# Kernel tuning notes

Hardware: AMD Instinct MI355X
Metric: run time of the kernel (lower is better)

## Reference

```python
import jax, jax.numpy as jnp
import numpy as np

W_LEN = 37  # window_length
EPS = 1e-9
LRELU_SLOPE = 0.2
SQRT2 = 1.4142135623730951


def win_sum(x, w):
    # Depthwise sliding-window sum of width w, 'same' padding w//2 (odd w).
    # Equivalent to the diag-kernel conv1d in the original code, but O(T) via cumsum.
    pad = w // 2
    xp = jnp.pad(x, ((0, 0), (0, 0), (pad, pad)))
    cs = jnp.cumsum(xp, axis=-1)
    cs = jnp.pad(cs, ((0, 0), (0, 0), (1, 0)))
    return cs[..., w:] - cs[..., :-w]


def conv1d(x, w, b):
    # x: [B,C,T], w: [O,I,3], padding=1
    y = jax.lax.conv_general_dilated(x, w, (1,), [(1, 1)],
                                     dimension_numbers=('NCH', 'OIH', 'NCH'))
    return y + b[None, :, None]


def adawin_instance(x, s, mask, fc_w, fc_b, alpha):
    # x: [B,C,T], s: [B,S,T], mask: [B,T]
    C = x.shape[1]
    h = jnp.einsum('bst,cs->bct', s, fc_w) + fc_b[None, :, None]  # [B,2C,T]
    m = mask[:, None, :]                       # [B,1,T]
    denom = win_sum(m, W_LEN) + EPS            # same for all channels
    gamma = win_sum(h[:, :C], W_LEN) / denom * m
    beta = win_sum(h[:, C:], W_LEN) / denom * m
    x_norm = jnp.tanh(alpha * x)               # WindowedNorm1d.forward
    return (1.0 + gamma) * x_norm + beta


def setup_inputs() -> dict:
    key = jax.random.key(0)
    ks = jax.random.split(key, 10)
    B, C_IN, C_OUT, S, T = 16, 512, 512, 128, 2048
    inp = {
        'x': jax.random.normal(ks[0], (B, C_IN, T), dtype=jnp.float32),
        's': jax.random.normal(ks[1], (B, S, T), dtype=jnp.float32),
        'lengths': jax.random.randint(ks[2], (B,), 0, T).astype(jnp.int32),
        'fc1_w': jax.random.normal(ks[3], (2 * C_IN, S), dtype=jnp.float32) * 0.05,
        'fc1_b': jnp.zeros((2 * C_IN,), dtype=jnp.float32),
        'alpha1': jnp.full((1,), 0.5, dtype=jnp.float32),
        'conv1_w': jax.random.normal(ks[4], (C_OUT, C_IN, 3), dtype=jnp.float32) * 0.02,
        'conv1_b': jnp.zeros((C_OUT,), dtype=jnp.float32),
        'fc2_w': jax.random.normal(ks[5], (2 * C_OUT, S), dtype=jnp.float32) * 0.05,
        'fc2_b': jnp.zeros((2 * C_OUT,), dtype=jnp.float32),
        'alpha2': jnp.full((1,), 0.5, dtype=jnp.float32),
        'conv2_w': jax.random.normal(ks[6], (C_OUT, C_OUT, 3), dtype=jnp.float32) * 0.02,
        'conv2_b': jnp.zeros((C_OUT,), dtype=jnp.float32),
    }
    return inp


def reference(x, s, lengths, fc1_w, fc1_b, alpha1, conv1_w, conv1_b,
              fc2_w, fc2_b, alpha2, conv2_w, conv2_b):
    T = x.shape[2]
    mask = (jnp.arange(T)[None, :] < lengths[:, None]).astype(x.dtype)  # [B,T]

    h = adawin_instance(x, s, mask, fc1_w, fc1_b, alpha1)
    h = jax.nn.leaky_relu(h, LRELU_SLOPE)
    h = conv1d(h, conv1_w, conv1_b)
    h = adawin_instance(h, s, mask, fc2_w, fc2_b, alpha2)
    h = jax.nn.leaky_relu(h, LRELU_SLOPE)
    h = conv1d(h, conv2_w, conv2_b)

    # dim_in == dim_out -> identity shortcut
    return (h + x) / SQRT2
```

## Files before the change

### kernel.cpp

```cpp
#include <hip/hip_runtime.h>

#define B_ 16
#define C_ 512
#define S_ 128
#define T_ 2048
#define HALF 18
#define WLEN 37

typedef __bf16 bf16x8 __attribute__((ext_vector_type(8)));
typedef float f32x4 __attribute__((ext_vector_type(4)));
typedef float f32x16 __attribute__((ext_vector_type(16)));
typedef unsigned short ushort_t;

__device__ inline ushort_t f2bf(float x) {
    unsigned u = __float_as_uint(x);
    u += 0x7fffu + ((u >> 16) & 1u);
    return (ushort_t)(u >> 16);
}
__device__ inline float bf2f(ushort_t h) {
    return __uint_as_float(((unsigned)h) << 16);
}
__device__ inline float fast_tanh(float z) {
    float e = __expf(2.f * z);
    return 1.f - __fdividef(2.f, e + 1.f);
}
__device__ __forceinline__ void glds16(const void* g, void* l) {
    __builtin_amdgcn_global_load_lds(
        (const __attribute__((address_space(1))) unsigned*)g,
        (__attribute__((address_space(3))) unsigned*)l, 16, 0, 0);
}

#define MFMA16(a, b, c) __builtin_amdgcn_mfma_f32_16x16x32_bf16((a), (b), (c), 0, 0, 0)
#define MFMA32(a, b, c) __builtin_amdgcn_mfma_f32_32x32x16_bf16((a), (b), (c), 0, 0, 0)

__global__ void prep_weights(const float* __restrict__ fc1, const float* __restrict__ fc2,
                             ushort_t* __restrict__ Wfc) {
    const int n_fc = 1024 * 128;
    int idx = blockIdx.x * blockDim.x + threadIdx.x;
    if (idx < n_fc) Wfc[idx] = f2bf(fc1[idx]);
    else if (idx < 2 * n_fc) Wfc[idx] = f2bf(fc2[idx - n_fc]);
}

#define IMGCH 53248
#define A_BYTES 53248
#define B_BYTES 22528
__global__ void prep_conv_images(const float* __restrict__ c1, const float* __restrict__ c2,
                                 ushort_t* __restrict__ I1, ushort_t* __restrict__ I2) {
    int idx = blockIdx.x * blockDim.x + threadIdx.x;
    const int per_conv = 2 * 16 * 256 * 13;
    if (idx >= 2 * per_conv) return;
    int conv = idx >= per_conv;
    int rr = conv ? idx - per_conv : idx;
    const float* src = conv ? c2 : c1;
    ushort_t* dst = conv ? I2 : I1;
    int imgchunk = rr / 3328;
    int rem = rr - imgchunk * 3328;
    int r = rem / 13;
    int g = rem - r * 13;
    int mb = imgchunk >> 4, ch = imgchunk & 15;
    ushort_t vals[8];
    if (g == 12) {
#pragma unroll
        for (int e = 0; e < 8; ++e) vals[e] = 0;
    } else {
        int tap = g >> 2, seg = g & 3;
        int o = mb * 256 + r;
        int chb = ch * 32 + seg * 8;
#pragma unroll
        for (int e = 0; e < 8; ++e)
            vals[e] = f2bf(src[(size_t)(o * 512 + chb + e) * 3 + tap]);
    }
    uint4 pk;
    pk.x = vals[0] | ((unsigned)vals[1] << 16);
    pk.y = vals[2] | ((unsigned)vals[3] << 16);
    pk.z = vals[4] | ((unsigned)vals[5] << 16);
    pk.w = vals[6] | ((unsigned)vals[7] << 16);
    *(uint4*)&dst[(size_t)rr * 8] = pk;
}

__global__ void zero_pads(ushort_t* __restrict__ y1p, ushort_t* __restrict__ y2p) {
    int tid = blockIdx.x * blockDim.x + threadIdx.x;
    if (tid < 4096) {
        ushort_t* base = (tid & 1) ? y2p : y1p;
        int r = tid >> 1;
        int bb = r >> 7;
        int rowsel = (r >> 6) & 1;
        int col = (r & 63) * 8;
        size_t row = (size_t)bb * (T_ + 2) + (rowsel ? (T_ + 1) : 0);
        *(uint4*)&base[row * C_ + col] = (uint4){0, 0, 0, 0};
    }
}

__global__ __launch_bounds__(256) void winsum_kernel(const float* __restrict__ s,
                                                     ushort_t* __restrict__ sw_t) {
    int b = blockIdx.y;
    int t0 = blockIdx.x * 64;
    __shared__ float sb[128][101];
    int tid = threadIdx.x;
    for (int e = tid; e < 128 * 100; e += 256) {
        int sj = e / 100;
        int u = e - sj * 100;
        int gt = t0 - HALF + u;
        float v = 0.f;
        if (gt >= 0 && gt < T_) v = s[((size_t)(b * S_ + sj)) * T_ + gt];
        sb[sj][u] = v;
    }
    __syncthreads();
    for (int e = tid; e < 64 * 128; e += 256) {
        int tl = e >> 7;
        int sj = e & 127;
        float sum = 0.f;
#pragma unroll
        for (int d = 0; d < WLEN; ++d) sum += sb[sj][tl + d];
        sw_t[((size_t)(b * T_ + t0 + tl)) * S_ + sj] = f2bf(sum);
    }
}

template <int INLAYOUT>
__global__ __launch_bounds__(256) void adawin_kernel(
    const void* __restrict__ xin_, const ushort_t* __restrict__ sw_t,
    const ushort_t* __restrict__ Wfc, const float* __restrict__ fcb,
    const float* __restrict__ alpha, const int* __restrict__ lengths,
    ushort_t* __restrict__ youtp) {
    int t0 = blockIdx.x * 64;
    int c0 = blockIdx.y * 64;
    int b = blockIdx.z;
    __shared__ __attribute__((aligned(16))) ushort_t smem[128 * 136 + 64 * 136];
    ushort_t (*As)[136] = (ushort_t(*)[136])smem;
    ushort_t (*Bs)[136] = (ushort_t(*)[136])(smem + 128 * 136);
    int tid = threadIdx.x;

    {
        int r = tid >> 4;
        int cseg = (tid & 15) * 8;
#pragma unroll
        for (int p = 0; p < 8; ++p) {
            int row = p * 16 + r;
            int grow = (row < 64) ? (c0 + row) : (448 + c0 + row);
            *(uint4*)&As[row][cseg] = *(const uint4*)&Wfc[(size_t)grow * 128 + cseg];
        }
    }
    {
        int tl = tid & 63;
        int sg = tid >> 6;
        const ushort_t* src = &sw_t[((size_t)(b * T_ + t0 + tl)) * S_];
#pragma unroll
        for (int j = 0; j < 4; ++j) {
            int col = sg * 32 + j * 8;
            *(uint4*)&Bs[tl][col] = *(const uint4*)&src[col];
        }
    }
    __syncthreads();

    int wave = tid >> 6, lane = tid & 63;
    int quad = lane >> 4, l = lane & 15;
    f32x4 accg[4], accb[4];
#pragma unroll
    for (int n = 0; n < 4; ++n) {
        accg[n] = (f32x4){0.f, 0.f, 0.f, 0.f};
        accb[n] = (f32x4){0.f, 0.f, 0.f, 0.f};
    }
    int rg = wave * 16 + l;
    int rb = 64 + wave * 16 + l;
#pragma unroll
    for (int ks = 0; ks < 4; ++ks) {
        int kc = ks * 32 + quad * 8;
        bf16x8 ag = *(const bf16x8*)&As[rg][kc];
        bf16x8 ab = *(const bf16x8*)&As[rb][kc];
#pragma unroll
        for (int n = 0; n < 4; ++n) {
            bf16x8 bb = *(const bf16x8*)&Bs[n * 16 + l][kc];
            accg[n] = MFMA16(ag, bb, accg[n]);
            accb[n] = MFMA16(ab, bb, accb[n]);
        }
    }

    __syncthreads();
    ushort_t (*Ts)[72] = (ushort_t(*)[72])smem;

    int len = lengths[b];
    float alph = alpha[0];
    const float* xf = (const float*)xin_;
    const ushort_t* xh = (const ushort_t*)xin_;
    int clocal = wave * 16 + quad * 4;
    int cbase = c0 + clocal;
#pragma unroll
    for (int n = 0; n < 4; ++n) {
        int t = t0 + n * 16 + l;
        int lo = t - HALF; if (lo < 0) lo = 0;
        int hi = t + HALF; if (hi > T_ - 1) hi = T_ - 1;
        float cnt = (float)(hi - lo + 1);
        int hv = hi < (len - 1) ? hi : (len - 1);
        int mdi = hv - lo + 1; if (mdi < 0) mdi = 0;
        float m = (t < len) ? 1.f : 0.f;
        float sc = m / ((float)mdi + 1e-9f);

        float xv[4];
        if (INLAYOUT == 0) {
#pragma unroll
            for (int j = 0; j < 4; ++j)
                xv[j] = xf[(size_t)(b * C_ + cbase + j) * T_ + t];
        } else {
            uint2 xraw = *(const uint2*)&xh[((size_t)(b * (T_ + 2) + 1 + t)) * C_ + cbase];
            xv[0] = bf2f((ushort_t)(xraw.x & 0xffff));
            xv[1] = bf2f((ushort_t)(xraw.x >> 16));
            xv[2] = bf2f((ushort_t)(xraw.y & 0xffff));
            xv[3] = bf2f((ushort_t)(xraw.y >> 16));
        }
        unsigned pk[2];
#pragma unroll
        for (int j = 0; j < 4; ++j) {
            int c = cbase + j;
            float gamma = (accg[n][j] + fcb[c] * cnt) * sc;
            float beta = (accb[n][j] + fcb[C_ + c] * cnt) * sc;
            float xn = fast_tanh(alph * xv[j]);
            float v = (1.f + gamma) * xn + beta;
            v = v > 0.f ? v : 0.2f * v;
            unsigned hv16 = (unsigned)f2bf(v);
            if (j & 1) pk[j >> 1] |= hv16 << 16;
            else pk[j >> 1] = hv16;
        }
        *(uint2*)&Ts[n * 16 + l][clocal] = (uint2){pk[0], pk[1]};
    }
    __syncthreads();
    {
        int row = tid >> 2;
        int seg = (tid & 3) * 16;
        size_t gbase = ((size_t)(b * (T_ + 2) + 1 + t0 + row)) * C_ + c0 + seg;
        *(uint4*)&youtp[gbase] = *(const uint4*)&Ts[row][seg];
        *(uint4*)&youtp[gbase + 8] = *(const uint4*)&Ts[row][seg + 8];
    }
}

__device__ __forceinline__ void issue_g(int g, const char* img, const char* xt, int ch,
                                        char* Ab, char* Bb, int lane) {
    if (g < 52) {
        glds16(img + g * 1024 + lane * 16, Ab + g * 1024);
    } else if (g < 74) {
        int j = g - 52;
        int gi = j * 64 + lane;
        int r = gi / 5;
        int gg = gi - r * 5;
        if (gg == 4) gg = 0;
        if (r > 257) r = 257;
        glds16(xt + (size_t)r * 1024 + ch * 64 + gg * 16, Bb + j * 1024);
    } else {
        int j = g - 74;
        glds16(img + j * 1024 + lane * 16, Ab + j * 1024);
    }
}
template <int G0, int G1>
__device__ __forceinline__ void issue_batch(const char* img, const char* xt, int ch,
                                            char* Ab, char* Bb, int wave, int lane) {
#pragma unroll
    for (int g = G0; g < G1; ++g) {
        if ((g & 7) != wave) continue;
        issue_g(g, img, xt, ch, Ab, Bb, lane);
    }
}

template <int EPI>
__global__ __launch_bounds__(512, 2) void conv_kernel(
    const ushort_t* __restrict__ Xp, const ushort_t* __restrict__ Wimg,
    const float* __restrict__ bias, const float* __restrict__ resid,
    ushort_t* __restrict__ out_bf, float* __restrict__ out_f) {
    int t0 = blockIdx.x * 256;
    int o0 = blockIdx.y * 256;
    int b = blockIdx.z;
    __shared__ __attribute__((aligned(16))) char smem[2 * A_BYTES + 2 * B_BYTES];
    int tid = threadIdx.x;
    int lane = tid & 63, wave = tid >> 6;
    int l32 = lane & 31, khalf = lane >> 5;
    int wm = wave >> 2, wn = wave & 3;

    const char* imgch = (const char*)Wimg + (size_t)blockIdx.y * 16 * IMGCH;
    const char* xt = (const char*)Xp + (size_t)(b * (T_ + 2) + t0) * 1024;

    f32x16 acc[4][2];
#pragma unroll
    for (int m = 0; m < 4; ++m)
#pragma unroll
        for (int nf = 0; nf < 2; ++nf)
#pragma unroll
            for (int r = 0; r < 16; ++r) acc[m][nf][r] = 0.f;

    char* A0 = smem;
    char* A1 = smem + A_BYTES;
    char* Bb0 = smem + 2 * A_BYTES;
    char* Bb1 = Bb0 + B_BYTES;

    issue_batch<0, 80>(imgch, xt, 0, A0, Bb0, wave, lane);
    issue_batch<0, 32>(imgch + IMGCH, xt, 1, A1, Bb1, wave, lane);
    asm volatile("s_waitcnt vmcnt(4)" ::: "memory");
    asm volatile("s_barrier" ::: "memory");

#pragma unroll 1
    for (int ch = 0; ch < 16; ++ch) {
        int cur = ch & 1;
        char* Ac = smem + cur * A_BYTES;
        char* Bc = smem + 2 * A_BYTES + cur * B_BYTES;
        char* An = smem + (cur ^ 1) * A_BYTES;
        char* Bn = smem + 2 * A_BYTES + (cur ^ 1) * B_BYTES;
        ushort_t (*As)[104] = (ushort_t(*)[104])Ac;
        ushort_t (*Bs)[40] = (ushort_t(*)[40])Bc;
        const char* img_n1 = imgch + (size_t)(ch + 1) * IMGCH;

#pragma unroll
        for (int p = 0; p < 3; ++p) {
            bf16x8 af[2][4], bf[2][2];
#pragma unroll
            for (int m = 0; m < 4; ++m) {
                const ushort_t* ar = &As[wm * 128 + m * 32 + l32][p * 32 + khalf * 8];
                af[0][m] = *(const bf16x8*)ar;
                af[1][m] = *(const bf16x8*)(ar + 16);
            }
#pragma unroll
            for (int nf = 0; nf < 2; ++nf) {
                const ushort_t* br = &Bs[wn * 64 + nf * 32 + l32 + p][khalf * 8];
                bf[0][nf] = *(const bf16x8*)br;
                bf[1][nf] = *(const bf16x8*)(br + 16);
            }
            if (ch < 15) {
                if (p == 0) issue_batch<32, 56>(img_n1, xt, ch + 1, An, Bn, wave, lane);
                else if (p == 1) issue_batch<56, 80>(img_n1, xt, ch + 1, An, Bn, wave, lane);
            }
            asm volatile("s_barrier" ::: "memory");
            asm volatile("s_waitcnt lgkmcnt(0)" ::: "memory");
            __builtin_amdgcn_sched_barrier(0);
            __builtin_amdgcn_s_setprio(1);
#pragma unroll
            for (int ks = 0; ks < 2; ++ks)
#pragma unroll
                for (int m = 0; m < 4; ++m)
#pragma unroll
                    for (int nf = 0; nf < 2; ++nf)
                        acc[m][nf] = MFMA32(af[ks][m], bf[ks][nf], acc[m][nf]);
            __builtin_amdgcn_s_setprio(0);
            asm volatile("s_barrier" ::: "memory");
        }
        if (ch < 14) {
            issue_batch<0, 32>(imgch + (size_t)(ch + 2) * IMGCH, xt, ch + 2, Ac, Bc,
                               wave, lane);
            asm volatile("s_waitcnt vmcnt(4)" ::: "memory");
            asm volatile("s_barrier" ::: "memory");
        } else if (ch == 14) {
            asm volatile("s_waitcnt vmcnt(0)" ::: "memory");
            asm volatile("s_barrier" ::: "memory");
        }
    }

    if (EPI == 0) {
        __syncthreads();
        ushort_t (*Ts)[264] = (ushort_t(*)[264])smem;
#pragma unroll
        for (int nf = 0; nf < 2; ++nf) {
            int trow = wn * 64 + nf * 32 + l32;
#pragma unroll
            for (int m = 0; m < 4; ++m) {
#pragma unroll
                for (int g = 0; g < 4; ++g) {
                    int oc = wm * 128 + m * 32 + g * 8 + khalf * 4;
                    unsigned pk[2];
#pragma unroll
                    for (int j = 0; j < 4; ++j) {
                        float v = acc[m][nf][g * 4 + j] + bias[o0 + oc + j];
                        unsigned hv16 = (unsigned)f2bf(v);
                        if (j & 1) pk[j >> 1] |= hv16 << 16;
                        else pk[j >> 1] = hv16;
                    }
                    *(uint2*)&Ts[trow][oc] = (uint2){pk[0], pk[1]};
                }
            }
        }
        __syncthreads();
        int row = tid >> 1;
        int colh = (tid & 1) * 128;
        size_t gbase = ((size_t)(b * (T_ + 2) + 1 + t0 + row)) * C_ + o0 + colh;
#pragma unroll
        for (int j = 0; j < 16; ++j)
            *(uint4*)&out_bf[gbase + j * 8] = *(const uint4*)&Ts[row][colh + j * 8];
    } else {
#pragma unroll
        for (int m = 0; m < 4; ++m)
#pragma unroll
            for (int nf = 0; nf < 2; ++nf) {
                int t = t0 + wn * 64 + nf * 32 + l32;
#pragma unroll
                for (int g = 0; g < 4; ++g) {
                    int oo = o0 + wm * 128 + m * 32 + g * 8 + khalf * 4;
#pragma unroll
                    for (int j = 0; j < 4; ++j) {
                        size_t off = (size_t)(b * C_ + oo + j) * T_ + t;
                        out_f[off] = (acc[m][nf][g * 4 + j] + bias[oo + j] + resid[off]) *
                                     0.70710678118654752f;
                    }
                }
            }
    }
}

extern "C" void kernel_launch(void* const* d_in, const int* in_sizes, int n_in,
                              void* d_out, int out_size, void* d_ws, size_t ws_size,
                              hipStream_t stream) {
    const float* x = (const float*)d_in[0];
    const float* s = (const float*)d_in[1];
    const int* lengths = (const int*)d_in[2];
    const float* fc1_w = (const float*)d_in[3];
    const float* fc1_b = (const float*)d_in[4];
    const float* alpha1 = (const float*)d_in[5];
    const float* conv1_w = (const float*)d_in[6];
    const float* conv1_b = (const float*)d_in[7];
    const float* fc2_w = (const float*)d_in[8];
    const float* fc2_b = (const float*)d_in[9];
    const float* alpha2 = (const float*)d_in[10];
    const float* conv2_w = (const float*)d_in[11];
    const float* conv2_b = (const float*)d_in[12];

    const size_t IMGB = (size_t)2 * 16 * IMGCH;
    char* ws = (char*)d_ws;
    ushort_t* sw_t = (ushort_t*)ws; ws += (size_t)B_ * T_ * S_ * 2;
    ushort_t* Wfc = (ushort_t*)ws;  ws += (size_t)2 * 1024 * 128 * 2;
    ushort_t* I1 = (ushort_t*)ws;   ws += IMGB;
    ushort_t* I2 = (ushort_t*)ws;   ws += IMGB;
    ushort_t* y2p = (ushort_t*)ws;  ws += (size_t)B_ * (T_ + 2) * C_ * 2;
    ushort_t* y1p = (ushort_t*)ws;  ws += (size_t)B_ * (T_ + 2) * C_ * 2;
    ws += 12 * 1024;
    if ((size_t)(ws - (char*)d_ws) > ws_size) return;

    prep_weights<<<dim3(1024), dim3(256), 0, stream>>>(fc1_w, fc2_w, Wfc);
    prep_conv_images<<<dim3(832), dim3(256), 0, stream>>>(conv1_w, conv2_w, I1, I2);
    winsum_kernel<<<dim3(32, 16), dim3(256), 0, stream>>>(s, sw_t);
    zero_pads<<<dim3(16), dim3(256), 0, stream>>>(y1p, y2p);
    adawin_kernel<0><<<dim3(32, 8, 16), dim3(256), 0, stream>>>(
        (const void*)x, sw_t, Wfc, fc1_b, alpha1, lengths, y1p);
    conv_kernel<0><<<dim3(8, 2, 16), dim3(512), 0, stream>>>(
        y1p, I1, conv1_b, (const float*)nullptr, y2p, (float*)nullptr);
    adawin_kernel<1><<<dim3(32, 8, 16), dim3(256), 0, stream>>>(
        (const void*)y2p, sw_t, Wfc + 1024 * 128, fc2_b, alpha2, lengths, y1p);
    conv_kernel<1><<<dim3(8, 2, 16), dim3(512), 0, stream>>>(
        y1p, I2, conv2_b, x, (ushort_t*)nullptr, (float*)d_out);
}
```

Measured before the change: 371.0 us.

## Restructure conv pipeline into smaller K-chunks with triple buffering; merge prep kernels

```diff
diff --git a/kernel.cpp b/kernel.cpp
--- a/kernel.cpp
+++ b/kernel.cpp
@@ -33,86 +33,88 @@
 #define MFMA16(a, b, c) __builtin_amdgcn_mfma_f32_16x16x32_bf16((a), (b), (c), 0, 0, 0)
 #define MFMA32(a, b, c) __builtin_amdgcn_mfma_f32_32x32x16_bf16((a), (b), (c), 0, 0, 0)
 
-__global__ void prep_weights(const float* __restrict__ fc1, const float* __restrict__ fc2,
-                             ushort_t* __restrict__ Wfc) {
-    const int n_fc = 1024 * 128;
-    int idx = blockIdx.x * blockDim.x + threadIdx.x;
-    if (idx < n_fc) Wfc[idx] = f2bf(fc1[idx]);
-    else if (idx < 2 * n_fc) Wfc[idx] = f2bf(fc2[idx - n_fc]);
-}
-
-#define IMGCH 53248
-#define A_BYTES 53248
-#define B_BYTES 22528
-__global__ void prep_conv_images(const float* __restrict__ c1, const float* __restrict__ c2,
-                                 ushort_t* __restrict__ I1, ushort_t* __restrict__ I2) {
-    int idx = blockIdx.x * blockDim.x + threadIdx.x;
-    const int per_conv = 2 * 16 * 256 * 13;
-    if (idx >= 2 * per_conv) return;
-    int conv = idx >= per_conv;
-    int rr = conv ? idx - per_conv : idx;
-    const float* src = conv ? c2 : c1;
-    ushort_t* dst = conv ? I2 : I1;
-    int imgchunk = rr / 3328;
-    int rem = rr - imgchunk * 3328;
-    int r = rem / 13;
-    int g = rem - r * 13;
-    int mb = imgchunk >> 4, ch = imgchunk & 15;
-    ushort_t vals[8];
-    if (g == 12) {
-#pragma unroll
-        for (int e = 0; e < 8; ++e) vals[e] = 0;
+#define ACH_BYTES 28672
+#define BCH_BYTES 13312
+#define CH_BYTES (ACH_BYTES + BCH_BYTES)
+
+__global__ __launch_bounds__(256) void prep_all(
+    const float* __restrict__ s, ushort_t* __restrict__ sw_t,
+    const float* __restrict__ fc1, const float* __restrict__ fc2,
+    ushort_t* __restrict__ Wfc, const float* __restrict__ c1,
+    const float* __restrict__ c2, ushort_t* __restrict__ I1,
+    ushort_t* __restrict__ I2, ushort_t* __restrict__ y1p,
+    ushort_t* __restrict__ y2p) {
+    __shared__ float sb[128][101];
+    int bid = blockIdx.x;
+    int tid = threadIdx.x;
+    if (bid < 512) {
+        int b = bid >> 5;
+        int t0 = (bid & 31) * 64;
+        for (int e = tid; e < 128 * 100; e += 256) {
+            int sj = e / 100;
+            int u = e - sj * 100;
+            int gt = t0 - HALF + u;
+            float v = 0.f;
+            if (gt >= 0 && gt < T_) v = s[((size_t)(b * S_ + sj)) * T_ + gt];
+            sb[sj][u] = v;
+        }
+        __syncthreads();
+        for (int e = tid; e < 64 * 128; e += 256) {
+            int tl = e >> 7;
+            int sj = e & 127;
+            float sum = 0.f;
+#pragma unroll
+            for (int d = 0; d < WLEN; ++d) sum += sb[sj][tl + d];
+            sw_t[((size_t)(b * T_ + t0 + tl)) * S_ + sj] = f2bf(sum);
+        }
+    } else if (bid < 1408) {
+        int idx = (bid - 512) * 256 + tid;
+        const int per_conv = 2 * 32 * 1792;
+        int conv = idx >= per_conv;
+        int rr = conv ? idx - per_conv : idx;
+        const float* src = conv ? c2 : c1;
+        ushort_t* dst = conv ? I2 : I1;
+        int chunk_id = rr / 1792;
+        int srem = rr - chunk_id * 1792;
+        int mb = chunk_id >> 5, cc = chunk_id & 31;
+        int off = srem * 16;
+        int row = off / 112;
+        int c = off - row * 112;
+        ushort_t vals[8];
+        if (c >= 96) {
+#pragma unroll
+            for (int e = 0; e < 8; ++e) vals[e] = 0;
+        } else {
+            int tap = c >> 5;
+            int ch_lo = (c & 31) >> 1;
+            int o = mb * 256 + row;
+            int ibase = cc * 16 + ch_lo;
+#pragma unroll
+            for (int e = 0; e < 8; ++e)
+                vals[e] = f2bf(src[(size_t)(o * 512 + ibase + e) * 3 + tap]);
+        }
+        uint4 pk;
+        pk.x = vals[0] | ((unsigned)vals[1] << 16);
+        pk.y = vals[2] | ((unsigned)vals[3] << 16);
+        pk.z = vals[4] | ((unsigned)vals[5] << 16);
+        pk.w = vals[6] | ((unsigned)vals[7] << 16);
+        *(uint4*)&dst[(size_t)rr * 8] = pk;
+    } else if (bid < 2432) {
+        const int n_fc = 1024 * 128;
+        int idx = (bid - 1408) * 256 + tid;
+        if (idx < n_fc) Wfc[idx] = f2bf(fc1[idx]);
+        else if (idx < 2 * n_fc) Wfc[idx] = f2bf(fc2[idx - n_fc]);
     } else {
-        int tap = g >> 2, seg = g & 3;
-        int o = mb * 256 + r;
-        int chb = ch * 32 + seg * 8;
-#pragma unroll
-        for (int e = 0; e < 8; ++e)
-            vals[e] = f2bf(src[(size_t)(o * 512 + chb + e) * 3 + tap]);
-    }
-    uint4 pk;
-    pk.x = vals[0] | ((unsigned)vals[1] << 16);
-    pk.y = vals[2] | ((unsigned)vals[3] << 16);
-    pk.z = vals[4] | ((unsigned)vals[5] << 16);
-    pk.w = vals[6] | ((unsigned)vals[7] << 16);
-    *(uint4*)&dst[(size_t)rr * 8] = pk;
-}
-
-__global__ void zero_pads(ushort_t* __restrict__ y1p, ushort_t* __restrict__ y2p) {
-    int tid = blockIdx.x * blockDim.x + threadIdx.x;
-    if (tid < 4096) {
-        ushort_t* base = (tid & 1) ? y2p : y1p;
-        int r = tid >> 1;
-        int bb = r >> 7;
-        int rowsel = (r >> 6) & 1;
-        int col = (r & 63) * 8;
-        size_t row = (size_t)bb * (T_ + 2) + (rowsel ? (T_ + 1) : 0);
-        *(uint4*)&base[row * C_ + col] = (uint4){0, 0, 0, 0};
-    }
-}
-
-__global__ __launch_bounds__(256) void winsum_kernel(const float* __restrict__ s,
-                                                     ushort_t* __restrict__ sw_t) {
-    int b = blockIdx.y;
-    int t0 = blockIdx.x * 64;
-    __shared__ float sb[128][101];
-    int tid = threadIdx.x;
-    for (int e = tid; e < 128 * 100; e += 256) {
-        int sj = e / 100;
-        int u = e - sj * 100;
-        int gt = t0 - HALF + u;
-        float v = 0.f;
-        if (gt >= 0 && gt < T_) v = s[((size_t)(b * S_ + sj)) * T_ + gt];
-        sb[sj][u] = v;
-    }
-    __syncthreads();
-    for (int e = tid; e < 64 * 128; e += 256) {
-        int tl = e >> 7;
-        int sj = e & 127;
-        float sum = 0.f;
-#pragma unroll
-        for (int d = 0; d < WLEN; ++d) sum += sb[sj][tl + d];
-        sw_t[((size_t)(b * T_ + t0 + tl)) * S_ + sj] = f2bf(sum);
+        int t2 = (bid - 2432) * 256 + tid;
+        if (t2 < 4096) {
+            ushort_t* base = (t2 & 1) ? y2p : y1p;
+            int r = t2 >> 1;
+            int bb = r >> 7;
+            int rowsel = (r >> 6) & 1;
+            int col = (r & 63) * 8;
+            size_t row = (size_t)bb * (T_ + 2) + (rowsel ? (T_ + 1) : 0);
+            *(uint4*)&base[row * C_ + col] = (uint4){0, 0, 0, 0};
+        }
     }
 }
 
@@ -232,30 +234,27 @@
     }
 }
 
-__device__ __forceinline__ void issue_g(int g, const char* img, const char* xt, int ch,
-                                        char* Ab, char* Bb, int lane) {
-    if (g < 52) {
-        glds16(img + g * 1024 + lane * 16, Ab + g * 1024);
-    } else if (g < 74) {
-        int j = g - 52;
-        int gi = j * 64 + lane;
-        int r = gi / 5;
-        int gg = gi - r * 5;
-        if (gg == 4) gg = 0;
-        if (r > 257) r = 257;
-        glds16(xt + (size_t)r * 1024 + ch * 64 + gg * 16, Bb + j * 1024);
-    } else {
-        int j = g - 74;
-        glds16(img + j * 1024 + lane * 16, Ab + j * 1024);
-    }
-}
-template <int G0, int G1>
-__device__ __forceinline__ void issue_batch(const char* img, const char* xt, int ch,
-                                            char* Ab, char* Bb, int wave, int lane) {
-#pragma unroll
-    for (int g = G0; g < G1; ++g) {
-        if ((g & 7) != wave) continue;
-        issue_g(g, img, xt, ch, Ab, Bb, lane);
+__device__ __forceinline__ void stage_chunk(const char* img, const char* xt, int cc,
+                                            char* buf, int wave, int lane) {
+    char* Ab = buf;
+    char* Bb = buf + ACH_BYTES;
+#pragma unroll
+    for (int k = 0; k < 6; ++k) {
+        int g = wave + 8 * k;
+        if (g < 28) {
+            glds16(img + g * 1024 + lane * 16, Ab + g * 1024);
+        } else if (g < 41) {
+            int j = g - 28;
+            int off = j * 1024 + lane * 16;
+            int r = off / 48;
+            int sl = (off - r * 48) >> 4;
+            if (sl == 2) sl = 0;
+            if (r > 257) r = 257;
+            glds16(xt + (size_t)r * 1024 + cc * 32 + sl * 16, Bb + j * 1024);
+        } else {
+            int j = g - 41;
+            glds16(img + j * 1024 + lane * 16, Ab + j * 1024);
+        }
     }
 }
 
@@ -267,13 +266,13 @@
     int t0 = blockIdx.x * 256;
     int o0 = blockIdx.y * 256;
     int b = blockIdx.z;
-    __shared__ __attribute__((aligned(16))) char smem[2 * A_BYTES + 2 * B_BYTES];
+    __shared__ __attribute__((aligned(16))) char smem[135168];
     int tid = threadIdx.x;
     int lane = tid & 63, wave = tid >> 6;
     int l32 = lane & 31, khalf = lane >> 5;
     int wm = wave >> 2, wn = wave & 3;
 
-    const char* imgch = (const char*)Wimg + (size_t)blockIdx.y * 16 * IMGCH;
+    const char* imgcc = (const char*)Wimg + (size_t)blockIdx.y * 32 * ACH_BYTES;
     const char* xt = (const char*)Xp + (size_t)(b * (T_ + 2) + t0) * 1024;
 
     f32x16 acc[4][2];
@@ -284,69 +283,41 @@
 #pragma unroll
             for (int r = 0; r < 16; ++r) acc[m][nf][r] = 0.f;
 
-    char* A0 = smem;
-    char* A1 = smem + A_BYTES;
-    char* Bb0 = smem + 2 * A_BYTES;
-    char* Bb1 = Bb0 + B_BYTES;
-
-    issue_batch<0, 80>(imgch, xt, 0, A0, Bb0, wave, lane);
-    issue_batch<0, 32>(imgch + IMGCH, xt, 1, A1, Bb1, wave, lane);
-    asm volatile("s_waitcnt vmcnt(4)" ::: "memory");
+    stage_chunk(imgcc, xt, 0, smem, wave, lane);
+    stage_chunk(imgcc + ACH_BYTES, xt, 1, smem + CH_BYTES, wave, lane);
+    asm volatile("s_waitcnt vmcnt(6)" ::: "memory");
     asm volatile("s_barrier" ::: "memory");
 
+    int cur = 0;
 #pragma unroll 1
-    for (int ch = 0; ch < 16; ++ch) {
-        int cur = ch & 1;
-        char* Ac = smem + cur * A_BYTES;
-        char* Bc = smem + 2 * A_BYTES + cur * B_BYTES;
-        char* An = smem + (cur ^ 1) * A_BYTES;
-        char* Bn = smem + 2 * A_BYTES + (cur ^ 1) * B_BYTES;
-        ushort_t (*As)[104] = (ushort_t(*)[104])Ac;
-        ushort_t (*Bs)[40] = (ushort_t(*)[40])Bc;
-        const char* img_n1 = imgch + (size_t)(ch + 1) * IMGCH;
-
+    for (int c = 0; c < 32; ++c) {
+        char* buf = smem + cur * CH_BYTES;
+        if (c + 2 < 32) {
+            int s2 = cur + 2; if (s2 >= 3) s2 -= 3;
+            stage_chunk(imgcc + (size_t)(c + 2) * ACH_BYTES, xt, c + 2,
+                        smem + s2 * CH_BYTES, wave, lane);
+        }
+        ushort_t (*As)[56] = (ushort_t(*)[56])buf;
+        ushort_t (*Bs)[24] = (ushort_t(*)[24])(buf + ACH_BYTES);
 #pragma unroll
         for (int p = 0; p < 3; ++p) {
-            bf16x8 af[2][4], bf[2][2];
-#pragma unroll
-            for (int m = 0; m < 4; ++m) {
-                const ushort_t* ar = &As[wm * 128 + m * 32 + l32][p * 32 + khalf * 8];
-                af[0][m] = *(const bf16x8*)ar;
-                af[1][m] = *(const bf16x8*)(ar + 16);
-            }
-#pragma unroll
-            for (int nf = 0; nf < 2; ++nf) {
-                const ushort_t* br = &Bs[wn * 64 + nf * 32 + l32 + p][khalf * 8];
-                bf[0][nf] = *(const bf16x8*)br;
-                bf[1][nf] = *(const bf16x8*)(br + 16);
-            }
-            if (ch < 15) {
-                if (p == 0) issue_batch<32, 56>(img_n1, xt, ch + 1, An, Bn, wave, lane);
-                else if (p == 1) issue_batch<56, 80>(img_n1, xt, ch + 1, An, Bn, wave, lane);
-            }
-            asm volatile("s_barrier" ::: "memory");
-            asm volatile("s_waitcnt lgkmcnt(0)" ::: "memory");
-            __builtin_amdgcn_sched_barrier(0);
-            __builtin_amdgcn_s_setprio(1);
-#pragma unroll
-            for (int ks = 0; ks < 2; ++ks)
-#pragma unroll
-                for (int m = 0; m < 4; ++m)
-#pragma unroll
-                    for (int nf = 0; nf < 2; ++nf)
-                        acc[m][nf] = MFMA32(af[ks][m], bf[ks][nf], acc[m][nf]);
-            __builtin_amdgcn_s_setprio(0);
-            asm volatile("s_barrier" ::: "memory");
-        }
-        if (ch < 14) {
-            issue_batch<0, 32>(imgch + (size_t)(ch + 2) * IMGCH, xt, ch + 2, Ac, Bc,
-                               wave, lane);
-            asm volatile("s_waitcnt vmcnt(4)" ::: "memory");
-            asm volatile("s_barrier" ::: "memory");
-        } else if (ch == 14) {
-            asm volatile("s_waitcnt vmcnt(0)" ::: "memory");
-            asm volatile("s_barrier" ::: "memory");
-        }
+            bf16x8 a[4], bv[2];
+#pragma unroll
+            for (int m = 0; m < 4; ++m)
+                a[m] = *(const bf16x8*)&As[wm * 128 + m * 32 + l32][p * 16 + khalf * 8];
+#pragma unroll
+            for (int nf = 0; nf < 2; ++nf)
+                bv[nf] = *(const bf16x8*)&Bs[wn * 64 + nf * 32 + l32 + p][khalf * 8];
+#pragma unroll
+            for (int m = 0; m < 4; ++m)
+#pragma unroll
+                for (int nf = 0; nf < 2; ++nf)
+                    acc[m][nf] = MFMA32(a[m], bv[nf], acc[m][nf]);
+        }
+        if (c + 2 < 32) asm volatile("s_waitcnt vmcnt(6)" ::: "memory");
+        else if (c + 1 < 32) asm volatile("s_waitcnt vmcnt(0)" ::: "memory");
+        asm volatile("s_barrier" ::: "memory");
+        cur = cur + 1; if (cur >= 3) cur = 0;
     }
 
     if (EPI == 0) {
@@ -416,7 +387,7 @@
     const float* conv2_w = (const float*)d_in[11];
     const float* conv2_b = (const float*)d_in[12];
 
-    const size_t IMGB = (size_t)2 * 16 * IMGCH;
+    const size_t IMGB = (size_t)2 * 32 * ACH_BYTES;
     char* ws = (char*)d_ws;
     ushort_t* sw_t = (ushort_t*)ws; ws += (size_t)B_ * T_ * S_ * 2;
     ushort_t* Wfc = (ushort_t*)ws;  ws += (size_t)2 * 1024 * 128 * 2;
@@ -427,10 +398,8 @@
     ws += 12 * 1024;
     if ((size_t)(ws - (char*)d_ws) > ws_size) return;
 
-    prep_weights<<<dim3(1024), dim3(256), 0, stream>>>(fc1_w, fc2_w, Wfc);
-    prep_conv_images<<<dim3(832), dim3(256), 0, stream>>>(conv1_w, conv2_w, I1, I2);
-    winsum_kernel<<<dim3(32, 16), dim3(256), 0, stream>>>(s, sw_t);
-    zero_pads<<<dim3(16), dim3(256), 0, stream>>>(y1p, y2p);
+    prep_all<<<dim3(2448), dim3(256), 0, stream>>>(
+        s, sw_t, fc1_w, fc2_w, Wfc, conv1_w, conv2_w, I1, I2, y1p, y2p);
     adawin_kernel<0><<<dim3(32, 8, 16), dim3(256), 0, stream>>>(
         (const void*)x, sw_t, Wfc, fc1_b, alpha1, lengths, y1p);
     conv_kernel<0><<<dim3(8, 2, 16), dim3(512), 0, stream>>>(
```

After: 347.1 us. -6.5%, faster.
